# Performance work log

Hardware: AMD Instinct MI355X
Metric: run time of the kernel (lower is better)

Reference implementation:

```python
import jax, jax.numpy as jnp
import numpy as np

B, N, M = 8, 8192, 2048
C1, C2 = 128, 256
H = 256  # mlp hidden/out channels


def setup_inputs() -> dict:
    key = jax.random.key(0)
    ks = jax.random.split(key, 8)
    return {
        "unknown": jax.random.normal(ks[0], (B, N, 3), dtype=jnp.float32),
        "known": jax.random.normal(ks[1], (B, M, 3), dtype=jnp.float32),
        "unknow_feats": jax.random.normal(ks[2], (B, C1, N), dtype=jnp.float32),
        "known_feats": jax.random.normal(ks[3], (B, C2, M), dtype=jnp.float32),
        "W1": jax.random.normal(ks[4], (H, C1 + C2), dtype=jnp.float32) * 0.02,
        "b1": jnp.zeros((H,), dtype=jnp.float32),
        "W2": jax.random.normal(ks[5], (H, H), dtype=jnp.float32) * 0.02,
        "b2": jnp.zeros((H,), dtype=jnp.float32),
    }


def _three_nn(unknown, known):
    # squared pairwise distances (B, n, m)
    d2 = jnp.sum((unknown[:, :, None, :] - known[:, None, :, :]) ** 2, axis=-1)
    neg_d2_top, idx = jax.lax.top_k(-d2, 3)  # 3 smallest distances
    dist = jnp.sqrt(jnp.maximum(-neg_d2_top, 0.0))  # (B, n, 3)
    return dist, idx


def _three_interpolate(features, idx, weight):
    # features: (B, c, m); idx, weight: (B, n, 3) -> (B, c, n)
    Bc, c, m = features.shape
    n = idx.shape[1]
    idx_flat = jnp.broadcast_to(idx.reshape(Bc, 1, n * 3), (Bc, c, n * 3))
    gathered = jnp.take_along_axis(features, idx_flat, axis=2).reshape(Bc, c, n, 3)
    return jnp.sum(gathered * weight[:, None, :, :], axis=-1)


def reference(unknown, known, unknow_feats, known_feats, W1, b1, W2, b2):
    dist, idx = _three_nn(unknown, known)
    dist_recip = 1.0 / (dist + 1e-8)
    weight = dist_recip / jnp.sum(dist_recip, axis=2, keepdims=True)  # (B, n, 3)
    interpolated = _three_interpolate(known_feats, idx, weight)  # (B, C2, n)
    new_features = jnp.concatenate([interpolated, unknow_feats], axis=1)  # (B, C1+C2, n)
    # shared MLP: two conv1x1 (bias, no BN) + ReLU
    h = jax.nn.relu(jnp.einsum('oc,bcn->bon', W1, new_features) + b1[None, :, None])
    out = jax.nn.relu(jnp.einsum('oc,bcn->bon', W2, h) + b2[None, :, None])
    return out
```

## Files before the change

kernel.cpp:

```cpp
#include <hip/hip_runtime.h>

using bf16x8 = __attribute__((ext_vector_type(8))) short;
using f32x4  = __attribute__((ext_vector_type(4))) float;
using f32x2  = __attribute__((ext_vector_type(2))) float;

constexpr int Bb = 8, Nn = 8192, Mm = 2048, C1 = 128, C2 = 256, Hh = 256, K1 = 384;
constexpr int KT1 = K1 / 32;
constexpr int KT2 = Hh / 32;
constexpr int RT = Hh / 16;
constexpr int NQ = 4;
constexpr int MQ = Mm / NQ;

__device__ __forceinline__ short f2bf(float x) {
  union { float f; unsigned u; } v; v.f = x;
  unsigned r = v.u + 0x7fff + ((v.u >> 16) & 1);
  return (short)(r >> 16);
}

__device__ __forceinline__ unsigned pk2bf(float a, float b) {
#if defined(__has_builtin) && __has_builtin(__builtin_amdgcn_cvt_pk_bf16_f32)
  typedef __attribute__((ext_vector_type(2))) __bf16 bf2_t;
  bf2_t r = __builtin_amdgcn_cvt_pk_bf16_f32(a, b);
  union { bf2_t v; unsigned u; } cvt; cvt.v = r;
  return cvt.u;
#else
  return (unsigned)(unsigned short)f2bf(a) | ((unsigned)(unsigned short)f2bf(b) << 16);
#endif
}

__device__ __forceinline__ float bflo(unsigned d) { return __uint_as_float(d << 16); }
__device__ __forceinline__ float bfhi(unsigned d) { return __uint_as_float(d & 0xffff0000u); }

__device__ __forceinline__ f32x2 pk_add(f32x2 a, f32x2 b) {
  f32x2 d; asm("v_pk_add_f32 %0, %1, %2" : "=v"(d) : "v"(a), "v"(b)); return d;
}
__device__ __forceinline__ f32x2 pk_mul(f32x2 a, f32x2 b) {
  f32x2 d; asm("v_pk_mul_f32 %0, %1, %2" : "=v"(d) : "v"(a), "v"(b)); return d;
}
__device__ __forceinline__ f32x2 pk_fma(f32x2 a, f32x2 b, f32x2 c) {
  f32x2 d; asm("v_pk_fma_f32 %0, %1, %2, %3" : "=v"(d) : "v"(a), "v"(b), "v"(c)); return d;
}

__device__ __forceinline__ void merge3(float a0, float a1, float a2, int A0, int A1, int A2,
                                       float b0, float b1, float b2, int B0, int B1, int B2,
                                       float& m0, float& m1, float& m2,
                                       int& j0, int& j1, int& j2) {
  bool ta = a0 <= b0;
  m0 = ta ? a0 : b0; j0 = ta ? A0 : B0;
  float na0 = ta ? a1 : a0, na1 = ta ? a2 : a1;
  int   nA0 = ta ? A1 : A0, nA1 = ta ? A2 : A1;
  float nb0 = ta ? b0 : b1, nb1 = ta ? b1 : b2;
  int   nB0 = ta ? B0 : B1, nB1 = ta ? B1 : B2;
  ta = na0 <= nb0;
  m1 = ta ? na0 : nb0; j1 = ta ? nA0 : nB0;
  float ma0 = ta ? na1 : na0; int mA0 = ta ? nA1 : nA0;
  float mb0 = ta ? nb0 : nb1; int mB0 = ta ? nB0 : nB1;
  ta = ma0 <= mb0;
  m2 = ta ? ma0 : mb0; j2 = ta ? mA0 : mB0;
}

__global__ __launch_bounds__(256) void prep_all_k(const float* __restrict__ kf,
                                                  short* __restrict__ kfTb,
                                                  const float* __restrict__ W1,
                                                  const float* __restrict__ W2,
                                                  short* __restrict__ W1f,
                                                  short* __restrict__ W2f) {
  __shared__ float tile[32][33];
  int bid = blockIdx.x, tid = threadIdx.x;
  if (bid < 4096) {
    int cx = bid & 63, ry = (bid >> 6) & 7, z = bid >> 9;
    const float* src = kf + (size_t)z * C2 * Mm;
    short* dst = kfTb + (size_t)z * Mm * C2;
    int c0 = cx * 32, r0 = ry * 32;
    int tx = tid & 31, ty = tid >> 5;
#pragma unroll
    for (int rr = ty; rr < 32; rr += 8)
      tile[rr][tx] = src[(size_t)(r0 + rr) * Mm + c0 + tx];
    __syncthreads();
#pragma unroll
    for (int cc = ty; cc < 32; cc += 8)
      dst[(size_t)(c0 + cc) * C2 + r0 + tx] = f2bf(tile[tx][cc]);
    return;
  }
  int id = (bid - 4096) * 256 + tid;
  const int n1 = KT1 * RT * 64;
  const int n2 = KT2 * RT * 64;
  if (id < n1) {
    int lane = id & 63, t = id >> 6;
    int kt = t / RT, rt = t % RT;
    int m = rt * 16 + (lane & 15), k0 = kt * 32 + (lane >> 4) * 8;
    bf16x8 f;
#pragma unroll
    for (int j = 0; j < 8; ++j) f[j] = f2bf(W1[(size_t)m * K1 + k0 + j]);
    *(bf16x8*)(W1f + (size_t)id * 8) = f;
  } else if (id < n1 + n2) {
    int id2 = id - n1;
    int lane = id2 & 63, t = id2 >> 6;
    int kt = t / RT, rt = t % RT;
    int m = rt * 16 + (lane & 15), k0 = kt * 32 + (lane >> 4) * 8;
    bf16x8 f;
#pragma unroll
    for (int j = 0; j < 8; ++j) f[j] = f2bf(W2[(size_t)m * Hh + k0 + j]);
    *(bf16x8*)(W2f + (size_t)id2 * 8) = f;
  }
}

__global__ __launch_bounds__(256) void nn_quarter_k(const float* __restrict__ unknown,
                                                    const float* __restrict__ known,
                                                    float* __restrict__ pd,
                                                    int* __restrict__ pi) {
  __shared__ float kx[MQ], ky[MQ], kz[MQ];
  int bid = blockIdx.x;
  int b = bid >> 7, rem = bid & 127;
  int q = rem & 3, nblk = rem >> 2;
  int n = nblk * 256 + threadIdx.x;
  const float* kb = known + ((size_t)b * Mm + q * MQ) * 3;
  for (int p = threadIdx.x; p < MQ; p += 256) {
    kx[p] = kb[3 * p]; ky[p] = kb[3 * p + 1]; kz[p] = kb[3 * p + 2];
  }
  __syncthreads();

  size_t ui = ((size_t)b * Nn + n) * 3;
  float ux = unknown[ui], uy = unknown[ui + 1], uz = unknown[ui + 2];
  float d0 = 1e30f, d1 = 1e30f, d2 = 1e30f;
  int i0 = 0, i1 = 0, i2 = 0;
  int gbase = q * MQ;

  f32x2 nux = { -ux, -ux }, nuy = { -uy, -uy }, nuz = { -uz, -uz };

#define NN_INS(dd, qq)                                                  \
  {                                                                     \
    if (__any((dd) < d2)) {  \
      int jm = gbase + jb + (qq);                                       \
      bool c0 = (dd) < d0, c1 = (dd) < d1, c2 = (dd) < d2;              \
      d2 = c1 ? d1 : (c2 ? (dd) : d2); i2 = c1 ? i1 : (c2 ? jm : i2);   \
      d1 = c0 ? d0 : (c1 ? (dd) : d1); i1 = c0 ? i0 : (c1 ? jm : i1);   \
      d0 = c0 ? (dd) : d0;             i0 = c0 ? jm : i0;               \
    }                                                                   \
  }

  const f32x2* kx2 = (const f32x2*)kx;
  const f32x2* ky2 = (const f32x2*)ky;
  const f32x2* kz2 = (const f32x2*)kz;
  for (int jb = 0; jb < MQ; jb += 4) {
    int h = jb >> 1;
    f32x2 xa = kx2[h], xb = kx2[h + 1];
    f32x2 ya = ky2[h], yb = ky2[h + 1];
    f32x2 za = kz2[h], zb = kz2[h + 1];
    f32x2 dxa = pk_add(xa, nux), dya = pk_add(ya, nuy), dza = pk_add(za, nuz);
    f32x2 dda = pk_fma(dza, dza, pk_fma(dya, dya, pk_mul(dxa, dxa)));
    f32x2 dxb = pk_add(xb, nux), dyb = pk_add(yb, nuy), dzb = pk_add(zb, nuz);
    f32x2 ddb = pk_fma(dzb, dzb, pk_fma(dyb, dyb, pk_mul(dxb, dxb)));
    NN_INS(dda.x, 0)
    NN_INS(dda.y, 1)
    NN_INS(ddb.x, 2)
    NN_INS(ddb.y, 3)
  }
#undef NN_INS

  size_t o = (((size_t)b * Nn + n) * NQ + q) * 3;
  pd[o] = d0; pd[o + 1] = d1; pd[o + 2] = d2;
  pi[o] = i0; pi[o + 1] = i1; pi[o + 2] = i2;
}

__global__ __launch_bounds__(256) void fused_gemm_k(
    const float* __restrict__ uf, const short* __restrict__ kfTb,
    const short* __restrict__ W1f, const float* __restrict__ b1,
    const short* __restrict__ W2f, const float* __restrict__ b2,
    const float* __restrict__ pd, const int* __restrict__ pi,
    float* __restrict__ out) {
  __shared__ short Fs[KT1 * 4 * 64 * 8];
  short* Hs = Fs;
  int bid = blockIdx.x;
  int b = bid >> 7, bt = bid & 127;
  int tid = threadIdx.x, lane = tid & 63, wv = tid >> 6;
  int quad = lane >> 4, col = lane & 15;

  {
    int n = bt * 64 + wv * 16 + col;
    size_t pbase = (size_t)(b * Nn + n) * (NQ * 3);
    float4 da = *(const float4*)&pd[pbase];
    float4 db = *(const float4*)&pd[pbase + 4];
    float4 dc = *(const float4*)&pd[pbase + 8];
    int4 ia = *(const int4*)&pi[pbase];
    int4 ib = *(const int4*)&pi[pbase + 4];
    int4 ic = *(const int4*)&pi[pbase + 8];
    float t0, t1, t2, u0, u1, u2, m0, m1, m2;
    int T0, T1, T2, U0, U1, U2, g0, g1, g2;
    merge3(da.x, da.y, da.z, ia.x, ia.y, ia.z,
           da.w, db.x, db.y, ia.w, ib.x, ib.y, t0, t1, t2, T0, T1, T2);
    merge3(db.z, db.w, dc.x, ib.z, ib.w, ic.x,
           dc.y, dc.z, dc.w, ic.y, ic.z, ic.w, u0, u1, u2, U0, U1, U2);
    merge3(t0, t1, t2, T0, T1, T2, u0, u1, u2, U0, U1, U2,
           m0, m1, m2, g0, g1, g2);
    float s0 = sqrtf(m0), s1 = sqrtf(m1), s2 = sqrtf(m2);
    float r0 = 1.f / (s0 + 1e-8f), r1 = 1.f / (s1 + 1e-8f), r2 = 1.f / (s2 + 1e-8f);
    float rs = 1.f / (r0 + r1 + r2);
    float w0 = r0 * rs, w1 = r1 * rs, w2 = r2 * rs;

    const short* kfb = kfTb + (size_t)b * Mm * C2;
#pragma unroll 4
    for (int kt = 0; kt < 8; ++kt) {
      int c0 = kt * 32 + quad * 8;
      uint4 q0 = *(const uint4*)&kfb[(size_t)g0 * C2 + c0];
      uint4 q1 = *(const uint4*)&kfb[(size_t)g1 * C2 + c0];
      uint4 q2 = *(const uint4*)&kfb[(size_t)g2 * C2 + c0];
      float e0 = w0 * bflo(q0.x) + w1 * bflo(q1.x) + w2 * bflo(q2.x);
      float e1 = w0 * bfhi(q0.x) + w1 * bfhi(q1.x) + w2 * bfhi(q2.x);
      float e2 = w0 * bflo(q0.y) + w1 * bflo(q1.y) + w2 * bflo(q2.y);
      float e3 = w0 * bfhi(q0.y) + w1 * bfhi(q1.y) + w2 * bfhi(q2.y);
      float e4 = w0 * bflo(q0.z) + w1 * bflo(q1.z) + w2 * bflo(q2.z);
      float e5 = w0 * bfhi(q0.z) + w1 * bfhi(q1.z) + w2 * bfhi(q2.z);
      float e6 = w0 * bflo(q0.w) + w1 * bflo(q1.w) + w2 * bflo(q2.w);
      float e7 = w0 * bfhi(q0.w) + w1 * bfhi(q1.w) + w2 * bfhi(q2.w);
      uint4 packed;
      packed.x = pk2bf(e0, e1); packed.y = pk2bf(e2, e3);
      packed.z = pk2bf(e4, e5); packed.w = pk2bf(e6, e7);
      *(uint4*)&Fs[((kt * 4 + wv) * 64 + lane) * 8] = packed;
    }
#pragma unroll 2
    for (int kt = 8; kt < 12; ++kt) {
      int c1 = (kt - 8) * 32 + quad * 8;
      float e[8];
#pragma unroll
      for (int j = 0; j < 8; ++j)
        e[j] = uf[((size_t)b * C1 + c1 + j) * Nn + n];
      uint4 packed;
      packed.x = pk2bf(e[0], e[1]); packed.y = pk2bf(e[2], e[3]);
      packed.z = pk2bf(e[4], e[5]); packed.w = pk2bf(e[6], e[7]);
      *(uint4*)&Fs[((kt * 4 + wv) * 64 + lane) * 8] = packed;
    }
  }
  __syncthreads();

  f32x4 acc[4][4];
#pragma unroll
  for (int r = 0; r < 4; ++r)
#pragma unroll
    for (int c = 0; c < 4; ++c) acc[r][c] = (f32x4){0.f, 0.f, 0.f, 0.f};

  for (int kt = 0; kt < KT1; ++kt) {
    bf16x8 Afr[4], Bfr[4];
#pragma unroll
    for (int r = 0; r < 4; ++r)
      Afr[r] = *(const bf16x8*)(W1f + ((size_t)(kt * RT + wv * 4 + r) * 64 + lane) * 8);
#pragma unroll
    for (int c = 0; c < 4; ++c)
      Bfr[c] = *(const bf16x8*)&Fs[((kt * 4 + c) * 64 + lane) * 8];
#pragma unroll
    for (int r = 0; r < 4; ++r)
#pragma unroll
      for (int c = 0; c < 4; ++c)
        acc[r][c] = __builtin_amdgcn_mfma_f32_16x16x32_bf16(Afr[r], Bfr[c], acc[r][c], 0, 0, 0);
  }
  __syncthreads();

#pragma unroll
  for (int r = 0; r < 4; ++r) {
    f32x4 bq = *(const f32x4*)&b1[wv * 64 + r * 16 + quad * 4];
#pragma unroll
    for (int c = 0; c < 4; ++c)
#pragma unroll
      for (int reg = 0; reg < 4; ++reg)
        acc[r][c][reg] = fmaxf(acc[r][c][reg] + bq[reg], 0.f);
  }
  {
    int addr_lo = (((quad & 1) * 2) * 16 + col) * 4;
    bool hiSel = lane >= 32;
#pragma unroll
    for (int ktl = 0; ktl < 2; ++ktl)
#pragma unroll
      for (int c = 0; c < 4; ++c) {
        float e[8];
#pragma unroll
        for (int j = 0; j < 8; ++j) {
          int addr = addr_lo + (j >> 2) * 64;
          int lo = __builtin_amdgcn_ds_bpermute(addr, __float_as_int(acc[ktl * 2][c][j & 3]));
          int hi = __builtin_amdgcn_ds_bpermute(addr, __float_as_int(acc[ktl * 2 + 1][c][j & 3]));
          e[j] = __int_as_float(hiSel ? hi : lo);
        }
        uint4 packed;
        packed.x = pk2bf(e[0], e[1]); packed.y = pk2bf(e[2], e[3]);
        packed.z = pk2bf(e[4], e[5]); packed.w = pk2bf(e[6], e[7]);
        *(uint4*)&Hs[(((wv * 2 + ktl) * 4 + c) * 64 + lane) * 8] = packed;
      }
  }
  __syncthreads();

  f32x4 acc2[4][4];
#pragma unroll
  for (int r = 0; r < 4; ++r)
#pragma unroll
    for (int c = 0; c < 4; ++c) acc2[r][c] = (f32x4){0.f, 0.f, 0.f, 0.f};

  for (int kt = 0; kt < KT2; ++kt) {
    bf16x8 Afr[4], Bfr[4];
#pragma unroll
    for (int r = 0; r < 4; ++r)
      Afr[r] = *(const bf16x8*)(W2f + ((size_t)(kt * RT + wv * 4 + r) * 64 + lane) * 8);
#pragma unroll
    for (int c = 0; c < 4; ++c)
      Bfr[c] = *(const bf16x8*)&Hs[((kt * 4 + c) * 64 + lane) * 8];
#pragma unroll
    for (int r = 0; r < 4; ++r)
#pragma unroll
      for (int c = 0; c < 4; ++c)
        acc2[r][c] = __builtin_amdgcn_mfma_f32_16x16x32_bf16(Afr[r], Bfr[c], acc2[r][c], 0, 0, 0);
  }

#pragma unroll
  for (int r = 0; r < 4; ++r) {
    f32x4 bq = *(const f32x4*)&b2[wv * 64 + r * 16 + quad * 4];
#pragma unroll
    for (int c = 0; c < 4; ++c)
#pragma unroll
      for (int reg = 0; reg < 4; ++reg) {
        int rowg = wv * 64 + r * 16 + quad * 4 + reg;
        int n = bt * 64 + c * 16 + col;
        out[((size_t)b * Hh + rowg) * Nn + n] = fmaxf(acc2[r][c][reg] + bq[reg], 0.f);
      }
  }
}

extern "C" void kernel_launch(void* const* d_in, const int* in_sizes, int n_in,
                              void* d_out, int out_size, void* d_ws, size_t ws_size,
                              hipStream_t stream) {
  const float* unknown = (const float*)d_in[0];
  const float* known   = (const float*)d_in[1];
  const float* uf      = (const float*)d_in[2];
  const float* kf      = (const float*)d_in[3];
  const float* W1      = (const float*)d_in[4];
  const float* b1      = (const float*)d_in[5];
  const float* W2      = (const float*)d_in[6];
  const float* b2      = (const float*)d_in[7];
  float* out = (float*)d_out;

  char* p = (char*)d_ws;
  short* kfTb = (short*)p; p += (size_t)Bb * Mm * C2 * 2;
  short* W1f = (short*)p;  p += (size_t)KT1 * RT * 64 * 8 * 2;
  short* W2f = (short*)p;  p += (size_t)KT2 * RT * 64 * 8 * 2;
  float* pd  = (float*)p;  p += (size_t)Bb * Nn * NQ * 3 * 4;
  int* pi    = (int*)p;    p += (size_t)Bb * Nn * NQ * 3 * 4;

  const int prep_blocks = 4096 + (KT1 * RT * 64 + KT2 * RT * 64 + 255) / 256;
  prep_all_k<<<dim3(prep_blocks), dim3(256), 0, stream>>>(kf, kfTb, W1, W2, W1f, W2f);
  nn_quarter_k<<<dim3(Bb * 32 * NQ), dim3(256), 0, stream>>>(unknown, known, pd, pi);
  fused_gemm_k<<<dim3(Bb * (Nn / 64)), dim3(256), 0, stream>>>(
      uf, kfTb, W1f, b1, W2f, b2, pd, pi, out);
}
```

Measured before the change: 217.1 us.

## Use branchless med3 top-3 distance pass followed by index-recovery pass in 3-NN

The 3-NN kernel is split into two passes over the shared-memory known points. The first keeps only the three smallest distances with a branchless fmin/med3 update. The second recomputes the distances and recovers the matching indices by comparing against those final values, and skips chunks where no lane has a candidate. This removes the divergent per-candidate index insertion and adds unrolling and launch bounds, at the cost of computing every distance twice. Ties may pick indices differently from the original ordering.

New measurement: 233.8 us. 1.08x slower.

```diff
diff --git a/kernel.cpp b/kernel.cpp
--- a/kernel.cpp
+++ b/kernel.cpp
@@ -39,6 +39,14 @@
 }
 __device__ __forceinline__ f32x2 pk_fma(f32x2 a, f32x2 b, f32x2 c) {
   f32x2 d; asm("v_pk_fma_f32 %0, %1, %2, %3" : "=v"(d) : "v"(a), "v"(b), "v"(c)); return d;
+}
+
+__device__ __forceinline__ float med3f(float a, float b, float c) {
+#if defined(__has_builtin) && __has_builtin(__builtin_amdgcn_fmed3f)
+  return __builtin_amdgcn_fmed3f(a, b, c);
+#else
+  return fmaxf(fminf(a, b), fminf(fmaxf(a, b), c));
+#endif
 }
 
 __device__ __forceinline__ void merge3(float a0, float a1, float a2, int A0, int A1, int A2,
@@ -105,58 +113,91 @@
   }
 }
 
-__global__ __launch_bounds__(256) void nn_quarter_k(const float* __restrict__ unknown,
-                                                    const float* __restrict__ known,
-                                                    float* __restrict__ pd,
-                                                    int* __restrict__ pi) {
+__global__ __launch_bounds__(256, 4) void nn_quarter_k(const float* __restrict__ unknown,
+                                                       const float* __restrict__ known,
+                                                       float* __restrict__ pd,
+                                                       int* __restrict__ pi) {
   __shared__ float kx[MQ], ky[MQ], kz[MQ];
   int bid = blockIdx.x;
   int b = bid >> 7, rem = bid & 127;
   int q = rem & 3, nblk = rem >> 2;
   int n = nblk * 256 + threadIdx.x;
+
+  size_t ui = ((size_t)b * Nn + n) * 3;
+  float ux = unknown[ui], uy = unknown[ui + 1], uz = unknown[ui + 2];
+
   const float* kb = known + ((size_t)b * Mm + q * MQ) * 3;
   for (int p = threadIdx.x; p < MQ; p += 256) {
     kx[p] = kb[3 * p]; ky[p] = kb[3 * p + 1]; kz[p] = kb[3 * p + 2];
   }
   __syncthreads();
 
-  size_t ui = ((size_t)b * Nn + n) * 3;
-  float ux = unknown[ui], uy = unknown[ui + 1], uz = unknown[ui + 2];
-  float d0 = 1e30f, d1 = 1e30f, d2 = 1e30f;
-  int i0 = 0, i1 = 0, i2 = 0;
-  int gbase = q * MQ;
-
   f32x2 nux = { -ux, -ux }, nuy = { -uy, -uy }, nuz = { -uz, -uz };
-
-#define NN_INS(dd, qq)                                                  \
-  {                                                                     \
-    if (__any((dd) < d2)) {  \
-      int jm = gbase + jb + (qq);                                       \
-      bool c0 = (dd) < d0, c1 = (dd) < d1, c2 = (dd) < d2;              \
-      d2 = c1 ? d1 : (c2 ? (dd) : d2); i2 = c1 ? i1 : (c2 ? jm : i2);   \
-      d1 = c0 ? d0 : (c1 ? (dd) : d1); i1 = c0 ? i0 : (c1 ? jm : i1);   \
-      d0 = c0 ? (dd) : d0;             i0 = c0 ? jm : i0;               \
-    }                                                                   \
-  }
 
   const f32x2* kx2 = (const f32x2*)kx;
   const f32x2* ky2 = (const f32x2*)ky;
   const f32x2* kz2 = (const f32x2*)kz;
-  for (int jb = 0; jb < MQ; jb += 4) {
+
+#define DIST2(X, Y, Z, DD)                                              \
+  f32x2 DD;                                                             \
+  {                                                                     \
+    f32x2 dx_ = pk_add((X), nux), dy_ = pk_add((Y), nuy),               \
+          dz_ = pk_add((Z), nuz);                                       \
+    DD = pk_fma(dz_, dz_, pk_fma(dy_, dy_, pk_mul(dx_, dx_)));          \
+  }
+
+  float d0 = 1e30f, d1 = 1e30f, d2 = 1e30f;
+#define UPD(dd)                                                         \
+  {                                                                     \
+    float t1_ = med3f(d0, d1, (dd));                                    \
+    float t2_ = med3f(d1, d2, (dd));                                    \
+    d0 = fminf(d0, (dd)); d1 = t1_; d2 = t2_;                           \
+  }
+  for (int jb = 0; jb < MQ; jb += 8) {
     int h = jb >> 1;
-    f32x2 xa = kx2[h], xb = kx2[h + 1];
-    f32x2 ya = ky2[h], yb = ky2[h + 1];
-    f32x2 za = kz2[h], zb = kz2[h + 1];
-    f32x2 dxa = pk_add(xa, nux), dya = pk_add(ya, nuy), dza = pk_add(za, nuz);
-    f32x2 dda = pk_fma(dza, dza, pk_fma(dya, dya, pk_mul(dxa, dxa)));
-    f32x2 dxb = pk_add(xb, nux), dyb = pk_add(yb, nuy), dzb = pk_add(zb, nuz);
-    f32x2 ddb = pk_fma(dzb, dzb, pk_fma(dyb, dyb, pk_mul(dxb, dxb)));
-    NN_INS(dda.x, 0)
-    NN_INS(dda.y, 1)
-    NN_INS(ddb.x, 2)
-    NN_INS(ddb.y, 3)
-  }
-#undef NN_INS
+    f32x2 xa = kx2[h],     ya = ky2[h],     za = kz2[h];
+    f32x2 xb = kx2[h + 1], yb = ky2[h + 1], zb = kz2[h + 1];
+    f32x2 xc = kx2[h + 2], yc = ky2[h + 2], zc = kz2[h + 2];
+    f32x2 xd = kx2[h + 3], yd = ky2[h + 3], zd = kz2[h + 3];
+    DIST2(xa, ya, za, dda)
+    DIST2(xb, yb, zb, ddb)
+    DIST2(xc, yc, zc, ddc)
+    DIST2(xd, yd, zd, ddd)
+    UPD(dda.x) UPD(dda.y) UPD(ddb.x) UPD(ddb.y)
+    UPD(ddc.x) UPD(ddc.y) UPD(ddd.x) UPD(ddd.y)
+  }
+#undef UPD
+
+  const float D0 = d0, D1 = d1, D2 = d2;
+  int i0 = -1, i1 = -1, i2 = -1;
+  int gbase = q * MQ;
+#define REC(dd, qq)                                                     \
+  {                                                                     \
+    if (__any((dd) <= D2)) {                                            \
+      int j_ = gbase + jb + (qq);                                       \
+      bool c0_ = (dd) <= D0 && i0 < 0;                                  \
+      bool c1_ = (dd) <= D1 && i1 < 0 && !c0_;                          \
+      bool c2_ = (dd) <= D2 && i2 < 0 && !c0_ && !c1_;                  \
+      i0 = c0_ ? j_ : i0;                                               \
+      i1 = c1_ ? j_ : i1;                                               \
+      i2 = c2_ ? j_ : i2;                                               \
+    }                                                                   \
+  }
+  for (int jb = 0; jb < MQ; jb += 8) {
+    int h = jb >> 1;
+    f32x2 xa = kx2[h],     ya = ky2[h],     za = kz2[h];
+    f32x2 xb = kx2[h + 1], yb = ky2[h + 1], zb = kz2[h + 1];
+    f32x2 xc = kx2[h + 2], yc = ky2[h + 2], zc = kz2[h + 2];
+    f32x2 xd = kx2[h + 3], yd = ky2[h + 3], zd = kz2[h + 3];
+    DIST2(xa, ya, za, dda)
+    DIST2(xb, yb, zb, ddb)
+    DIST2(xc, yc, zc, ddc)
+    DIST2(xd, yd, zd, ddd)
+    REC(dda.x, 0) REC(dda.y, 1) REC(ddb.x, 2) REC(ddb.y, 3)
+    REC(ddc.x, 4) REC(ddc.y, 5) REC(ddd.x, 6) REC(ddd.y, 7)
+  }
+#undef REC
+#undef DIST2
 
   size_t o = (((size_t)b * Nn + n) * NQ + q) * 3;
   pd[o] = d0; pd[o + 1] = d1; pd[o + 2] = d2;
```
